# Kernel tuning notes

Measured on AMD Instinct MI355X. Metric: run time of the kernel, lower is better.

Reference implementation:

```python
import jax, jax.numpy as jnp
import numpy as np

T = 128          # number_of_trees
B = 1024         # batch_size
D = 28 * 28      # hardcoded feature dim
K = 200          # hardcoded top-k


def setup_inputs() -> dict:
    key = jax.random.key(0)
    k1, k2 = jax.random.split(key)
    x = jax.random.normal(k1, (B, D), dtype=jnp.float32)
    attention_mask = jax.random.uniform(k2, (T, D), dtype=jnp.float32, minval=-1.0, maxval=1.0)
    return {"x": x, "attention_mask": attention_mask}


def reference(x, attention_mask):
    # sigmoid -> top-k -> scatter builds a sparse per-tree mask [T, D]
    att = jax.nn.sigmoid(attention_mask)                      # [T, D]
    topk, idx = jax.lax.top_k(att, K)                         # [T, K] each
    rows = jnp.arange(T)[:, None]                             # [T, 1]
    attention = jnp.zeros((T, D), dtype=att.dtype).at[rows, idx].set(topk)  # [T, D]
    # per-tree broadcast multiply, vectorized (replaces python loop over trees)
    xf = x.reshape(-1, D)                                     # [B, D]
    return_value = xf[:, None, :] * attention[None, :, :]     # [B, T, D]
    return (return_value, attention)
```

## Files before the change

kernel.cpp:

```cpp
#include <hip/hip_runtime.h>
#include <math.h>

#define NT 128
#define NB 1024
#define ND 784
#define NK 200
#define ND4 196
#define UB 7

typedef float vfloat4 __attribute__((ext_vector_type(4)));

__global__ __launch_bounds__(256) void topk_attention_kernel(
    const float* __restrict__ mask, float* __restrict__ att_out)
{
    __shared__ int wsum[32][4];
    __shared__ int wtie[4][4];

    const int t    = blockIdx.x;
    const int tid  = threadIdx.x;
    const int wave = tid >> 6;
    const int lane = tid & 63;

    unsigned int key[4];
    float        val[4];
    #pragma unroll
    for (int j = 0; j < 4; ++j) {
        const int d = tid + j * 256;
        if (d < ND) {
            const float f = mask[t * ND + d];
            const unsigned int b = __float_as_uint(f);
            key[j] = ((int)b < 0) ? ~b : (b | 0x80000000u);
            val[j] = 1.0f / (1.0f + expf(-f));
        } else { key[j] = 0u; val[j] = 0.0f; }
    }

    unsigned int p = 0;
    int need = NK;
    for (int bit = 31; bit >= 0; --bit) {
        const unsigned int test = (p >> bit) | 1u;
        int c = 0;
        #pragma unroll
        for (int j = 0; j < 4; ++j) c += ((key[j] >> bit) == test) ? 1 : 0;
        #pragma unroll
        for (int off = 32; off > 0; off >>= 1) c += __shfl_down(c, off);
        if (lane == 0) wsum[bit][wave] = c;
        __syncthreads();
        const int tot = wsum[bit][0] + wsum[bit][1] + wsum[bit][2] + wsum[bit][3];
        if (tot >= need) p |= (1u << bit);
        else             need -= tot;
    }

    int rankw[4];
    #pragma unroll
    for (int j = 0; j < 4; ++j) {
        const bool tie = (key[j] == p);
        const unsigned long long m = __ballot(tie);
        rankw[j] = __popcll(m & ((1ull << lane) - 1ull));
        if (lane == 0) wtie[j][wave] = __popcll(m);
    }
    __syncthreads();
    int jbase[4];
    {
        int pre = 0;
        #pragma unroll
        for (int j = 0; j < 4; ++j) {
            jbase[j] = pre;
            pre += wtie[j][0] + wtie[j][1] + wtie[j][2] + wtie[j][3];
        }
    }

    #pragma unroll
    for (int j = 0; j < 4; ++j) {
        const int d = tid + j * 256;
        if (d < ND) {
            bool keep = key[j] > p;
            if (key[j] == p) {
                int off = jbase[j] + rankw[j];
                for (int w = 0; w < 4; ++w) if (w < wave) off += wtie[j][w];
                keep = off < need;
            }
            att_out[t * ND + d] = keep ? val[j] : 0.0f;
        }
    }
}

__global__ __launch_bounds__(256) void bcast_mul_kernel(
    const vfloat4* __restrict__ x4, const vfloat4* __restrict__ att4,
    vfloat4* __restrict__ out4)
{
    __shared__ vfloat4 sx[ND4];
    const int b   = blockIdx.x;
    const int tid = threadIdx.x;
    if (tid < ND4) sx[tid] = x4[b * ND4 + tid];
    __syncthreads();

    vfloat4* __restrict__ outb = out4 + (size_t)b * (NT * ND4);

    vfloat4 cur[UB];
    #pragma unroll
    for (int u = 0; u < UB; ++u) cur[u] = att4[tid + u * 256];

    int d4 = (tid >= ND4) ? tid - ND4 : tid;

    for (int nb = 0; nb < 13; ++nb) {
        vfloat4 nxt[UB];
        const int kb = nb * UB;
        #pragma unroll
        for (int u = 0; u < UB; ++u) nxt[u] = att4[tid + (kb + UB + u) * 256];
        #pragma unroll
        for (int u = 0; u < UB; ++u) {
            const vfloat4 o = cur[u] * sx[d4];
            __builtin_nontemporal_store(o, &outb[tid + (kb + u) * 256]);
            d4 += 60; if (d4 >= ND4) d4 -= ND4;
        }
        #pragma unroll
        for (int u = 0; u < UB; ++u) cur[u] = nxt[u];
    }
    #pragma unroll
    for (int u = 0; u < UB; ++u) {
        const vfloat4 o = cur[u] * sx[d4];
        __builtin_nontemporal_store(o, &outb[tid + (13 * UB + u) * 256]);
        d4 += 60; if (d4 >= ND4) d4 -= ND4;
    }
}

extern "C" void kernel_launch(void* const* d_in, const int* in_sizes, int n_in,
                              void* d_out, int out_size, void* d_ws, size_t ws_size,
                              hipStream_t stream)
{
    (void)in_sizes; (void)n_in; (void)out_size; (void)d_ws; (void)ws_size;
    const float* x    = (const float*)d_in[0];
    const float* mask = (const float*)d_in[1];
    float* out = (float*)d_out;
    float* att = out + (size_t)NB * NT * ND;

    topk_attention_kernel<<<NT, 256, 0, stream>>>(mask, att);
    bcast_mul_kernel<<<NB, 256, 0, stream>>>(
        (const vfloat4*)x, (const vfloat4*)att, (vfloat4*)out);
}
```

Measured before the change: 421.5 us.

## Process four batch rows per block to reuse attention loads

```diff
diff --git a/kernel.cpp b/kernel.cpp
--- a/kernel.cpp
+++ b/kernel.cpp
@@ -7,6 +7,9 @@
 #define NK 200
 #define ND4 196
 #define UB 7
+#define RR 4
+#define TPB2 512
+#define TND4 (NT * ND4)
 
 typedef float vfloat4 __attribute__((ext_vector_type(4)));
 
@@ -84,43 +87,56 @@
     }
 }
 
-__global__ __launch_bounds__(256) void bcast_mul_kernel(
+__global__ __launch_bounds__(TPB2) void bcast_mul_kernel(
     const vfloat4* __restrict__ x4, const vfloat4* __restrict__ att4,
     vfloat4* __restrict__ out4)
 {
-    __shared__ vfloat4 sx[ND4];
-    const int b   = blockIdx.x;
+    __shared__ vfloat4 sx[RR * ND4];
+    const int b0  = blockIdx.x * RR;
     const int tid = threadIdx.x;
-    if (tid < ND4) sx[tid] = x4[b * ND4 + tid];
+
+    sx[tid] = x4[(size_t)b0 * ND4 + tid];
+    if (tid < RR * ND4 - TPB2)
+        sx[tid + TPB2] = x4[(size_t)b0 * ND4 + tid + TPB2];
     __syncthreads();
 
-    vfloat4* __restrict__ outb = out4 + (size_t)b * (NT * ND4);
+    vfloat4* __restrict__ outb = out4 + (size_t)b0 * TND4 + tid;
 
     vfloat4 cur[UB];
     #pragma unroll
-    for (int u = 0; u < UB; ++u) cur[u] = att4[tid + u * 256];
+    for (int u = 0; u < UB; ++u) cur[u] = att4[tid + u * TPB2];
 
-    int d4 = (tid >= ND4) ? tid - ND4 : tid;
+    int d4 = tid;
+    if (d4 >= 2 * ND4) d4 -= 2 * ND4;
+    else if (d4 >= ND4) d4 -= ND4;
 
-    for (int nb = 0; nb < 13; ++nb) {
+    for (int nb = 0; nb < 6; ++nb) {
         vfloat4 nxt[UB];
         const int kb = nb * UB;
         #pragma unroll
-        for (int u = 0; u < UB; ++u) nxt[u] = att4[tid + (kb + UB + u) * 256];
+        for (int u = 0; u < UB; ++u) nxt[u] = att4[tid + (kb + UB + u) * TPB2];
         #pragma unroll
         for (int u = 0; u < UB; ++u) {
-            const vfloat4 o = cur[u] * sx[d4];
-            __builtin_nontemporal_store(o, &outb[tid + (kb + u) * 256]);
-            d4 += 60; if (d4 >= ND4) d4 -= ND4;
+            const int k = kb + u;
+            #pragma unroll
+            for (int r = 0; r < RR; ++r) {
+                const vfloat4 o = cur[u] * sx[r * ND4 + d4];
+                __builtin_nontemporal_store(o, &outb[(size_t)r * TND4 + k * TPB2]);
+            }
+            d4 += 120; if (d4 >= ND4) d4 -= ND4;
         }
         #pragma unroll
         for (int u = 0; u < UB; ++u) cur[u] = nxt[u];
     }
     #pragma unroll
     for (int u = 0; u < UB; ++u) {
-        const vfloat4 o = cur[u] * sx[d4];
-        __builtin_nontemporal_store(o, &outb[tid + (13 * UB + u) * 256]);
-        d4 += 60; if (d4 >= ND4) d4 -= ND4;
+        const int k = 6 * UB + u;
+        #pragma unroll
+        for (int r = 0; r < RR; ++r) {
+            const vfloat4 o = cur[u] * sx[r * ND4 + d4];
+            __builtin_nontemporal_store(o, &outb[(size_t)r * TND4 + k * TPB2]);
+        }
+        d4 += 120; if (d4 >= ND4) d4 -= ND4;
     }
 }
 
@@ -135,6 +151,6 @@
     float* att = out + (size_t)NB * NT * ND;
 
     topk_attention_kernel<<<NT, 256, 0, stream>>>(mask, att);
-    bcast_mul_kernel<<<NB, 256, 0, stream>>>(
+    bcast_mul_kernel<<<NB / RR, TPB2, 0, stream>>>(
         (const vfloat4*)x, (const vfloat4*)att, (vfloat4*)out);
 }
```

Result: no change. 424.6 us (+0.7%).

## Split broadcast multiply into a 2D grid with two outputs per thread

Applied to the files above, without the earlier changes.

```diff
diff --git a/kernel.cpp b/kernel.cpp
--- a/kernel.cpp
+++ b/kernel.cpp
@@ -6,7 +6,8 @@
 #define ND 784
 #define NK 200
 #define ND4 196
-#define UB 7
+#define TND4 (NT * ND4)
+#define HALF4 (TND4 / 2)
 
 typedef float vfloat4 __attribute__((ext_vector_type(4)));
 
@@ -88,40 +89,18 @@
     const vfloat4* __restrict__ x4, const vfloat4* __restrict__ att4,
     vfloat4* __restrict__ out4)
 {
-    __shared__ vfloat4 sx[ND4];
-    const int b   = blockIdx.x;
-    const int tid = threadIdx.x;
-    if (tid < ND4) sx[tid] = x4[b * ND4 + tid];
-    __syncthreads();
+    const int b = blockIdx.y;
+    const int k = blockIdx.x * 256 + threadIdx.x;
+    const unsigned int t = (unsigned int)k / 196u;
+    const int d4 = k - (int)(t * 196u);
 
-    vfloat4* __restrict__ outb = out4 + (size_t)b * (NT * ND4);
+    const vfloat4 xs = x4[b * ND4 + d4];
+    const vfloat4 a0 = att4[k];
+    const vfloat4 a1 = att4[k + HALF4];
 
-    vfloat4 cur[UB];
-    #pragma unroll
-    for (int u = 0; u < UB; ++u) cur[u] = att4[tid + u * 256];
-
-    int d4 = (tid >= ND4) ? tid - ND4 : tid;
-
-    for (int nb = 0; nb < 13; ++nb) {
-        vfloat4 nxt[UB];
-        const int kb = nb * UB;
-        #pragma unroll
-        for (int u = 0; u < UB; ++u) nxt[u] = att4[tid + (kb + UB + u) * 256];
-        #pragma unroll
-        for (int u = 0; u < UB; ++u) {
-            const vfloat4 o = cur[u] * sx[d4];
-            __builtin_nontemporal_store(o, &outb[tid + (kb + u) * 256]);
-            d4 += 60; if (d4 >= ND4) d4 -= ND4;
-        }
-        #pragma unroll
-        for (int u = 0; u < UB; ++u) cur[u] = nxt[u];
-    }
-    #pragma unroll
-    for (int u = 0; u < UB; ++u) {
-        const vfloat4 o = cur[u] * sx[d4];
-        __builtin_nontemporal_store(o, &outb[tid + (13 * UB + u) * 256]);
-        d4 += 60; if (d4 >= ND4) d4 -= ND4;
-    }
+    vfloat4* __restrict__ ob = out4 + (size_t)b * TND4 + k;
+    ob[0]     = a0 * xs;
+    ob[HALF4] = a1 * xs;
 }
 
 extern "C" void kernel_launch(void* const* d_in, const int* in_sizes, int n_in,
@@ -135,6 +114,6 @@
     float* att = out + (size_t)NB * NT * ND;
 
     topk_attention_kernel<<<NT, 256, 0, stream>>>(mask, att);
-    bcast_mul_kernel<<<NB, 256, 0, stream>>>(
+    bcast_mul_kernel<<<dim3(HALF4 / 256, NB), 256, 0, stream>>>(
         (const vfloat4*)x, (const vfloat4*)att, (vfloat4*)out);
 }
```

New measurement: 436.1 us. +3.5%, slower.
